# Kernel tuning notes

Hardware: AMD Instinct MI355X
Metric: run time of the kernel (lower is better)

## Reference

```python
import jax, jax.numpy as jnp
import numpy as np

B, S, D, H = 2, 2048, 1024, 16
HD = D // H  # head_size = 64

def setup_inputs() -> dict:
    key = jax.random.key(0)
    ks = jax.random.split(key, 8)
    sc = 0.02
    return {
        "q": jax.random.normal(ks[0], (B, S, D), jnp.float32),
        "k": jax.random.normal(ks[1], (B, S, D), jnp.float32),
        "v": jax.random.normal(ks[2], (B, S, D), jnp.float32),
        "padding_mask": jnp.zeros((B, 1, 1, S), jnp.float32),
        "Wq": jax.random.normal(ks[3], (D, D), jnp.float32) * sc,
        "bq": jnp.zeros((D,), jnp.float32),
        "Wk": jax.random.normal(ks[4], (D, D), jnp.float32) * sc,
        "bk": jnp.zeros((D,), jnp.float32),
        "Wv": jax.random.normal(ks[5], (D, D), jnp.float32) * sc,
        "bv": jnp.zeros((D,), jnp.float32),
        "Wo": jax.random.normal(ks[6], (D, D), jnp.float32) * sc,
        "bo": jnp.zeros((D,), jnp.float32),
    }

def reference(q, k, v, padding_mask, Wq, bq, Wk, bk, Wv, bv, Wo, bo):
    b = q.shape[0]
    qh = (q @ Wq + bq).reshape(b, -1, H, HD)
    kh = (k @ Wk + bk).reshape(b, -1, H, HD)
    vh = (v @ Wv + bv).reshape(b, -1, H, HD)
    # [B, H, Sq, Sk] scores, materialized as in the original
    qk = jnp.einsum('bjhd,bkhd->bhjk', qh, kh) / jnp.sqrt(jnp.float32(HD))
    qk = qk + padding_mask * -1e12
    attn = jax.nn.softmax(qk, axis=-1)
    qkv = jnp.einsum('bhjk,bkhd->bjhd', attn, vh).reshape(b, -1, D)
    return qkv @ Wo + bo
```

## Files before the change

### kernel.cpp

```cpp
#include <hip/hip_runtime.h>
#include <math.h>

typedef __bf16 bf16_t;
typedef __bf16 bf16x8 __attribute__((ext_vector_type(8)));
typedef __bf16 bf16x4v __attribute__((ext_vector_type(4)));
typedef float f32x4 __attribute__((ext_vector_type(4)));
typedef float f32x16 __attribute__((ext_vector_type(16)));

#define LOG2E 1.4426950408889634f
#define MBIAS_C (-1e12f * LOG2E)

#if __has_builtin(__builtin_amdgcn_exp2f)
#define EXP2F(x) __builtin_amdgcn_exp2f(x)
#else
#define EXP2F(x) exp2f(x)
#endif

typedef __attribute__((address_space(1))) const unsigned int g_u32;
typedef __attribute__((address_space(3))) unsigned int l_u32;
__device__ __forceinline__ void load_lds_16B(const void* g, void* l){
  __builtin_amdgcn_global_load_lds((g_u32*)g, (l_u32*)l, 16, 0, 0);
}

__device__ __forceinline__ f32x16 zero16(){
  f32x16 z;
  #pragma unroll
  for (int i = 0; i < 16; i++) z[i] = 0.f;
  return z;
}

__global__ __launch_bounds__(256) void cast3_kernel(const float* __restrict__ q,
                                                    const float* __restrict__ k,
                                                    const float* __restrict__ v,
                                                    bf16_t* __restrict__ out){
  int z = blockIdx.y;
  const float* x = (z == 0) ? q : (z == 1) ? k : v;
  int i = blockIdx.x * 256 + threadIdx.x;
  float4 f = reinterpret_cast<const float4*>(x)[i];
  bf16x4v w;
  w[0] = (bf16_t)f.x; w[1] = (bf16_t)f.y; w[2] = (bf16_t)f.z; w[3] = (bf16_t)f.w;
  reinterpret_cast<bf16x4v*>(out + (size_t)z * 4194304)[i] = w;
}

__global__ __launch_bounds__(256) void wtrans4_kernel(const float* __restrict__ Wq,
                                                      const float* __restrict__ Wk,
                                                      const float* __restrict__ Wv,
                                                      const float* __restrict__ Wo,
                                                      bf16_t* __restrict__ Wcat,
                                                      bf16_t* __restrict__ Wot){
  __shared__ float T[32][33];
  int z = blockIdx.z;
  const float* W = (z == 0) ? Wq : (z == 1) ? Wk : (z == 2) ? Wv : Wo;
  bf16_t* dst = (z < 3) ? (Wcat + (size_t)z * 1024 * 1024) : Wot;
  int x = threadIdx.x, y = threadIdx.y;
  int k0 = blockIdx.y * 32, n0 = blockIdx.x * 32;
  #pragma unroll
  for (int i = 0; i < 4; i++) T[y + 8*i][x] = W[(size_t)(k0 + y + 8*i) * 1024 + n0 + x];
  __syncthreads();
  #pragma unroll
  for (int i = 0; i < 4; i++) dst[(size_t)(n0 + y + 8*i) * 1024 + k0 + x] = (bf16_t)T[x][y + 8*i];
}

__device__ __forceinline__ void qkv_epilogue(f32x4 (&acc)[4][4], int seg, int n0g, int m0,
                                             int wm, int wn, int l16, int lq,
                                             const float* bias, bf16_t* qp, bf16_t* kp,
                                             bf16_t* Vt){
  if (seg < 2){
    bf16_t* Cp = (seg == 0) ? qp : kp;
    float scale = (seg == 0) ? 0.125f * LOG2E : 1.0f;
    #pragma unroll
    for (int ti = 0; ti < 4; ti++){
      #pragma unroll
      for (int tj = 0; tj < 4; tj++){
        int col = (n0g + wn + tj*16 + l16) & 1023;
        float bvv = bias[col];
        #pragma unroll
        for (int r = 0; r < 4; r++){
          int row = m0 + wm + ti*16 + lq*4 + r;
          Cp[(size_t)row * 1024 + col] = (bf16_t)((acc[ti][tj][r] + bvv) * scale);
        }
      }
    }
  } else {
    #pragma unroll
    for (int ti = 0; ti < 4; ti++){
      #pragma unroll
      for (int tj = 0; tj < 4; tj++){
        int dg = (n0g - 2048) + wn + tj*16 + l16;
        int h = dg >> 6, dl = dg & 63;
        float bvv = bias[dg];
        #pragma unroll
        for (int r = 0; r < 4; r++){
          int row = m0 + wm + ti*16 + lq*4 + r;
          int b = row >> 11, s = row & 2047;
          Vt[(size_t)((b*16 + h)*64 + dl) * 2048 + s] = (bf16_t)(acc[ti][tj][r] + bvv);
        }
      }
    }
  }
}

__global__ __launch_bounds__(256) void gemm_qkv_bf(const bf16_t* __restrict__ qkvin,
                                                   const bf16_t* __restrict__ Wcat,
                                                   const float* __restrict__ bq,
                                                   const float* __restrict__ bk,
                                                   const float* __restrict__ bv,
                                                   bf16_t* __restrict__ qp,
                                                   bf16_t* __restrict__ kp,
                                                   bf16_t* __restrict__ Vt){
  const int K = 1024;
  __shared__ __align__(16) bf16_t As[128*32];
  __shared__ __align__(16) bf16_t Bs[128*32];
  int tid = threadIdx.x, wave = tid >> 6, lane = tid & 63;
  int l16 = lane & 15, lq = lane >> 4;
  int n0g = blockIdx.x * 128;
  int seg = n0g >> 10;
  const bf16_t* A   = qkvin + (size_t)seg * 4194304;
  const float* bias = (seg == 0) ? bq : (seg == 1) ? bk : bv;
  int m0 = blockIdx.y * 128;
  int wm = (wave >> 1) * 64, wn = (wave & 1) * 64;
  int cposR = lq ^ ((l16 >> 2) & 3);
  f32x4 acc[4][4] = {};
  for (int kt = 0; kt < K; kt += 32){
    __syncthreads();
    #pragma unroll
    for (int i = 0; i < 2; i++){
      int u = tid + 256*i;
      int r = u >> 2, cpos = u & 3, cg = cpos ^ ((r >> 2) & 3);
      int ldsoff = (wave*64 + 256*i) * 16;
      load_lds_16B(&A[(size_t)(m0 + r) * K + kt + cg*8], (char*)As + ldsoff);
      load_lds_16B(&Wcat[(size_t)(n0g + r) * K + kt + cg*8], (char*)Bs + ldsoff);
    }
    __syncthreads();
    bf16x8 af[4], bfr[4];
    #pragma unroll
    for (int t = 0; t < 4; t++) af[t]  = *reinterpret_cast<bf16x8*>(&As[(wm + t*16 + l16)*32 + cposR*8]);
    #pragma unroll
    for (int t = 0; t < 4; t++) bfr[t] = *reinterpret_cast<bf16x8*>(&Bs[(wn + t*16 + l16)*32 + cposR*8]);
    #pragma unroll
    for (int ti = 0; ti < 4; ti++)
      #pragma unroll
      for (int tj = 0; tj < 4; tj++)
        acc[ti][tj] = __builtin_amdgcn_mfma_f32_16x16x32_bf16(af[ti], bfr[tj], acc[ti][tj], 0, 0, 0);
  }
  qkv_epilogue(acc, seg, n0g, m0, wm, wn, l16, lq, bias, qp, kp, Vt);
}

__global__ __launch_bounds__(256) void gemm_qkv_f32(const float* __restrict__ qi,
                                                    const float* __restrict__ ki,
                                                    const float* __restrict__ vi,
                                                    const bf16_t* __restrict__ Wcat,
                                                    const float* __restrict__ bq,
                                                    const float* __restrict__ bk,
                                                    const float* __restrict__ bv,
                                                    bf16_t* __restrict__ qp,
                                                    bf16_t* __restrict__ kp,
                                                    bf16_t* __restrict__ Vt){
  const int K = 1024;
  __shared__ __align__(16) float  Asf[128*32];
  __shared__ __align__(16) bf16_t Bs[128*32];
  int tid = threadIdx.x, wave = tid >> 6, lane = tid & 63;
  int l16 = lane & 15, lq = lane >> 4;
  int n0g = blockIdx.x * 128;
  int seg = n0g >> 10;
  const float* A    = (seg == 0) ? qi : (seg == 1) ? ki : vi;
  const float* bias = (seg == 0) ? bq : (seg == 1) ? bk : bv;
  int m0 = blockIdx.y * 128;
  int wm = (wave >> 1) * 64, wn = (wave & 1) * 64;
  int cposR = lq ^ ((l16 >> 2) & 3);
  int ca0 = (2*lq)     ^ (l16 & 7);
  int ca1 = (2*lq + 1) ^ (l16 & 7);
  f32x4 acc[4][4] = {};
  for (int kt = 0; kt < K; kt += 32){
    __syncthreads();
    #pragma unroll
    for (int i = 0; i < 4; i++){
      int u = tid + 256*i;
      int r = u >> 3, cpos = u & 7, cg = cpos ^ (r & 7);
      load_lds_16B(&A[(size_t)(m0 + r) * K + kt + cg*4], (char*)Asf + (wave*64 + 256*i)*16);
    }
    #pragma unroll
    for (int i = 0; i < 2; i++){
      int u = tid + 256*i;
      int r = u >> 2, cpos = u & 3, cg = cpos ^ ((r >> 2) & 3);
      load_lds_16B(&Wcat[(size_t)(n0g + r) * K + kt + cg*8], (char*)Bs + (wave*64 + 256*i)*16);
    }
    __syncthreads();
    bf16x8 af[4], bfr[4];
    #pragma unroll
    for (int t = 0; t < 4; t++){
      int row = wm + t*16 + l16;
      f32x4 x0 = *reinterpret_cast<f32x4*>(&Asf[row*32 + ca0*4]);
      f32x4 x1 = *reinterpret_cast<f32x4*>(&Asf[row*32 + ca1*4]);
      bf16x8 a;
      a[0] = (bf16_t)x0[0]; a[1] = (bf16_t)x0[1]; a[2] = (bf16_t)x0[2]; a[3] = (bf16_t)x0[3];
      a[4] = (bf16_t)x1[0]; a[5] = (bf16_t)x1[1]; a[6] = (bf16_t)x1[2]; a[7] = (bf16_t)x1[3];
      af[t] = a;
    }
    #pragma unroll
    for (int t = 0; t < 4; t++) bfr[t] = *reinterpret_cast<bf16x8*>(&Bs[(wn + t*16 + l16)*32 + cposR*8]);
    #pragma unroll
    for (int ti = 0; ti < 4; ti++)
      #pragma unroll
      for (int tj = 0; tj < 4; tj++)
        acc[ti][tj] = __builtin_amdgcn_mfma_f32_16x16x32_bf16(af[ti], bfr[tj], acc[ti][tj], 0, 0, 0);
  }
  qkv_epilogue(acc, seg, n0g, m0, wm, wn, l16, lq, bias, qp, kp, Vt);
}

__global__ __launch_bounds__(256) void gemm_out(const bf16_t* __restrict__ A,
                                                const bf16_t* __restrict__ Bt,
                                                const float* __restrict__ bias,
                                                float* __restrict__ C){
  const int K = 1024, N = 1024;
  __shared__ __align__(16) bf16_t As[128*64];
  __shared__ __align__(16) bf16_t Bs[64*64];
  int tid = threadIdx.x, wave = tid >> 6, lane = tid & 63;
  int l16 = lane & 15, lq = lane >> 4;
  int m0 = blockIdx.y * 128, n0 = blockIdx.x * 64;
  int wm = wave * 32;
  f32x4 acc[2][4] = {};
  for (int kt = 0; kt < K; kt += 64){
    __syncthreads();
    #pragma unroll
    for (int i = 0; i < 4; i++){
      int u = tid + 256*i;
      int r = u >> 3, cpos = u & 7, cg = cpos ^ (r & 7);
      load_lds_16B(&A[(size_t)(m0 + r) * K + kt + cg*8], (char*)As + (wave*64 + 256*i)*16);
    }
    #pragma unroll
    for (int i = 0; i < 2; i++){
      int u = tid + 256*i;
      int r = u >> 3, cpos = u & 7, cg = cpos ^ (r & 7);
      load_lds_16B(&Bt[(size_t)(n0 + r) * K + kt + cg*8], (char*)Bs + (wave*64 + 256*i)*16);
    }
    __syncthreads();
    #pragma unroll
    for (int kk = 0; kk < 2; kk++){
      bf16x8 af[2], bfr[4];
      #pragma unroll
      for (int t = 0; t < 2; t++){
        int row = wm + t*16 + l16, cpos = (kk*4 + lq) ^ (l16 & 7);
        af[t] = *reinterpret_cast<bf16x8*>(&As[row*64 + cpos*8]);
      }
      #pragma unroll
      for (int t = 0; t < 4; t++){
        int row = t*16 + l16, cpos = (kk*4 + lq) ^ (l16 & 7);
        bfr[t] = *reinterpret_cast<bf16x8*>(&Bs[row*64 + cpos*8]);
      }
      #pragma unroll
      for (int ti = 0; ti < 2; ti++)
        #pragma unroll
        for (int tj = 0; tj < 4; tj++)
          acc[ti][tj] = __builtin_amdgcn_mfma_f32_16x16x32_bf16(af[ti], bfr[tj], acc[ti][tj], 0, 0, 0);
    }
  }
  #pragma unroll
  for (int ti = 0; ti < 2; ti++){
    #pragma unroll
    for (int tj = 0; tj < 4; tj++){
      int col = n0 + tj*16 + l16;
      float bvv = bias[col];
      #pragma unroll
      for (int r = 0; r < 4; r++){
        int row = m0 + wm + ti*16 + lq*4 + r;
        C[(size_t)row * N + col] = acc[ti][tj][r] + bvv;
      }
    }
  }
}

__global__ __launch_bounds__(256) void attn_kernel(const bf16_t* __restrict__ qp,
                                                   const bf16_t* __restrict__ kp,
                                                   const bf16_t* __restrict__ vt,
                                                   const float* __restrict__ mask,
                                                   bf16_t* __restrict__ ctx){
  const int S = 2048, D = 1024, HD = 64;
  __shared__ __align__(16) char smem[26624];
  bf16_t* Qs   = (bf16_t*)smem;
  bf16_t* Ps   = (bf16_t*)smem;
  bf16_t* Ks   = (bf16_t*)(smem + 10240);
  bf16_t* Vts  = (bf16_t*)(smem + 18432);
  float* Opart = (float*)smem;
  float* Lsum  = (float*)(smem + 16384);
  float* Lcomb = (float*)(smem + 16640);
  int tid = threadIdx.x, wave = tid >> 6, lane = tid & 63;
  int l32 = lane & 31, H = lane >> 5;
  int qhalf = wave & 1, khalf = wave >> 1;
  int qt = blockIdx.x, h = blockIdx.y, b = blockIdx.z;
  const bf16_t* Qg = qp + (size_t)b*S*D + h*HD;
  const bf16_t* Kg = kp + (size_t)b*S*D + h*HD;
  const bf16_t* Vg = vt + (size_t)(b*16 + h)*HD*S;

  #pragma unroll
  for (int i = 0; i < 2; i++){
    int u = tid + 256*i;
    int r = u >> 3, c = u & 7, cg = c ^ (r & 7);
    load_lds_16B(&Qg[(size_t)(qt*64 + r) * D + cg*8], smem + (wave*64 + 256*i)*16);
  }
  __syncthreads();
  int qrow = qhalf*32 + l32;
  bf16x8 qf[4];
  #pragma unroll
  for (int s = 0; s < 4; s++){
    int c = 2*s + H;
    qf[s] = *reinterpret_cast<bf16x8*>(&Qs[qrow*64 + (c ^ (qrow & 7))*8]);
  }
  f32x16 o0 = zero16(), o1 = zero16();
  float lacc = 0.f;
  int krow = khalf*32 + l32;
  bf16_t* Pw = Ps + wave*32*40;

  for (int kt = 0; kt < S; kt += 64){
    __syncthreads();
    #pragma unroll
    for (int i = 0; i < 2; i++){
      int u = tid + 256*i;
      int r = u >> 3, c = u & 7, cg = c ^ (r & 7);
      load_lds_16B(&Kg[(size_t)(kt + r) * D + cg*8], (char*)Ks + (wave*64 + 256*i)*16);
    }
    #pragma unroll
    for (int i = 0; i < 2; i++){
      int u = tid + 256*i;
      int r = u >> 3, c = u & 7, cg = c ^ (r & 7);
      load_lds_16B(&Vg[(size_t)r * S + kt + cg*8], (char*)Vts + (wave*64 + 256*i)*16);
    }
    __syncthreads();

    f32x16 sc;
    #pragma unroll
    for (int s = 0; s < 4; s++){
      int c = 2*s + H;
      bf16x8 kf = *reinterpret_cast<bf16x8*>(&Ks[krow*64 + (c ^ (krow & 7))*8]);
      if (s == 0) sc = __builtin_amdgcn_mfma_f32_32x32x16_bf16(kf, qf[0], zero16(), 0, 0, 0);
      else        sc = __builtin_amdgcn_mfma_f32_32x32x16_bf16(kf, qf[s], sc, 0, 0, 0);
    }
    float lt = 0.f;
    #pragma unroll
    for (int g = 0; g < 4; g++){
      int kcol = kt + khalf*32 + 8*g + 4*H;
      float4 mv = *reinterpret_cast<const float4*>(&mask[(size_t)b*S + kcol]);
      float p0 = EXP2F(fmaf(mv.x, MBIAS_C, sc[4*g+0]));
      float p1 = EXP2F(fmaf(mv.y, MBIAS_C, sc[4*g+1]));
      float p2 = EXP2F(fmaf(mv.z, MBIAS_C, sc[4*g+2]));
      float p3 = EXP2F(fmaf(mv.w, MBIAS_C, sc[4*g+3]));
      lt += (p0 + p1) + (p2 + p3);
      bf16x4v w;
      w[0] = (bf16_t)p0; w[1] = (bf16_t)p1; w[2] = (bf16_t)p2; w[3] = (bf16_t)p3;
      *reinterpret_cast<bf16x4v*>(&Pw[l32*40 + 8*g + 4*H]) = w;
    }
    lt += __shfl_xor(lt, 32);
    lacc += lt;
    #pragma unroll
    for (int ks = 0; ks < 2; ks++){
      bf16x8 pf = *reinterpret_cast<bf16x8*>(&Pw[l32*40 + ks*16 + 8*H]);
      int c0 = 4*khalf + 2*ks + H;
      bf16x8 vf0 = *reinterpret_cast<bf16x8*>(&Vts[l32*64 + (c0 ^ (l32 & 7))*8]);
      bf16x8 vf1 = *reinterpret_cast<bf16x8*>(&Vts[(32 + l32)*64 + (c0 ^ (l32 & 7))*8]);
      o0 = __builtin_amdgcn_mfma_f32_32x32x16_bf16(pf, vf0, o0, 0, 0, 0);
      o1 = __builtin_amdgcn_mfma_f32_32x32x16_bf16(pf, vf1, o1, 0, 0, 0);
    }
  }
  __syncthreads();
  if (khalf == 1){
    #pragma unroll
    for (int reg = 0; reg < 16; reg++){
      Opart[qhalf*2048 + reg*64 + lane]        = o0[reg];
      Opart[qhalf*2048 + 1024 + reg*64 + lane] = o1[reg];
    }
    Lsum[qhalf*32 + l32] = lacc;
  }
  __syncthreads();
  if (khalf == 0){
    #pragma unroll
    for (int reg = 0; reg < 16; reg++){
      o0[reg] += Opart[qhalf*2048 + reg*64 + lane];
      o1[reg] += Opart[qhalf*2048 + 1024 + reg*64 + lane];
    }
    lacc += Lsum[qhalf*32 + l32];
    Lcomb[qhalf*32 + l32] = lacc;
    #pragma unroll
    for (int g = 0; g < 4; g++){
      f32x4 lv = *reinterpret_cast<f32x4*>(&Lcomb[qhalf*32 + 8*g + 4*H]);
      #pragma unroll
      for (int j = 0; j < 4; j++){
        float inv = 1.f / lv[j];
        int grow = qt*64 + qhalf*32 + 8*g + 4*H + j;
        size_t base = (size_t)(b*S + grow) * D + h*HD;
        ctx[base + l32]      = (bf16_t)(o0[4*g + j] * inv);
        ctx[base + 32 + l32] = (bf16_t)(o1[4*g + j] * inv);
      }
    }
  }
}

extern "C" void kernel_launch(void* const* d_in, const int* in_sizes, int n_in,
                              void* d_out, int out_size, void* d_ws, size_t ws_size,
                              hipStream_t stream){
  const float* q    = (const float*)d_in[0];
  const float* k    = (const float*)d_in[1];
  const float* v    = (const float*)d_in[2];
  const float* mask = (const float*)d_in[3];
  const float* Wq   = (const float*)d_in[4];
  const float* bq   = (const float*)d_in[5];
  const float* Wk   = (const float*)d_in[6];
  const float* bk   = (const float*)d_in[7];
  const float* Wv   = (const float*)d_in[8];
  const float* bv   = (const float*)d_in[9];
  const float* Wo   = (const float*)d_in[10];
  const float* bo   = (const float*)d_in[11];

  char* ws = (char*)d_ws;
  bf16_t* qp    = (bf16_t*)(ws);
  bf16_t* kp    = (bf16_t*)(ws + 8388608);
  bf16_t* Vt    = (bf16_t*)(ws + 16777216);
  bf16_t* Wcat  = (bf16_t*)(ws + 25165824);
  bf16_t* Wot   = (bf16_t*)(ws + 31457280);
  bf16_t* ctx   = (bf16_t*)(ws + 33554432);
  bf16_t* qkvin = (bf16_t*)(ws + 33554432);

  wtrans4_kernel<<<dim3(32,32,4), dim3(32,8), 0, stream>>>(Wq, Wk, Wv, Wo, Wcat, Wot);
  if (ws_size >= 58720256){
    cast3_kernel<<<dim3(4096,3), 256, 0, stream>>>(q, k, v, qkvin);
    gemm_qkv_bf<<<dim3(24,32), 256, 0, stream>>>(qkvin, Wcat, bq, bk, bv, qp, kp, Vt);
  } else {
    gemm_qkv_f32<<<dim3(24,32), 256, 0, stream>>>(q, k, v, Wcat, bq, bk, bv, qp, kp, Vt);
  }
  attn_kernel<<<dim3(32,16,2), 256, 0, stream>>>(qp, kp, Vt, mask, ctx);
  gemm_out<<<dim3(16,32), 256, 0, stream>>>(ctx, Wot, bo, (float*)d_out);
}
```

Baseline: 268.7 us.

## Restructure attention to 128-row Q tiles with register-resident P and separate V transpose

The attention kernel now gives each wave 32 query rows against the full 64-key tile, instead of splitting keys across wave pairs. This removes the cross-wave O reduction through LDS, and P is rebuilt in registers with lane shuffles instead of a round trip through LDS. Q fragments load straight from global memory, and the grid halves to 16 query tiles of 128 rows. The scattered transposed V store in the QKV GEMM epilogue is replaced by a plain row-major store followed by a new LDS-tiled transpose kernel. That adds an extra launch and an extra pass over V in exchange for coalesced writes, and the fewer, larger attention blocks may lower occupancy.

```diff
diff --git a/kernel.cpp b/kernel.cpp
--- a/kernel.cpp
+++ b/kernel.cpp
@@ -28,6 +28,9 @@
   for (int i = 0; i < 16; i++) z[i] = 0.f;
   return z;
 }
+
+typedef union { bf16x4v b4; uint2 u2; } pk8;
+typedef union { uint2 h[2]; bf16x8 b8; } pk16;
 
 __global__ __launch_bounds__(256) void cast3_kernel(const float* __restrict__ q,
                                                     const float* __restrict__ k,
@@ -64,37 +67,19 @@
 __device__ __forceinline__ void qkv_epilogue(f32x4 (&acc)[4][4], int seg, int n0g, int m0,
                                              int wm, int wn, int l16, int lq,
                                              const float* bias, bf16_t* qp, bf16_t* kp,
-                                             bf16_t* Vt){
-  if (seg < 2){
-    bf16_t* Cp = (seg == 0) ? qp : kp;
-    float scale = (seg == 0) ? 0.125f * LOG2E : 1.0f;
-    #pragma unroll
-    for (int ti = 0; ti < 4; ti++){
-      #pragma unroll
-      for (int tj = 0; tj < 4; tj++){
-        int col = (n0g + wn + tj*16 + l16) & 1023;
-        float bvv = bias[col];
-        #pragma unroll
-        for (int r = 0; r < 4; r++){
-          int row = m0 + wm + ti*16 + lq*4 + r;
-          Cp[(size_t)row * 1024 + col] = (bf16_t)((acc[ti][tj][r] + bvv) * scale);
-        }
-      }
-    }
-  } else {
-    #pragma unroll
-    for (int ti = 0; ti < 4; ti++){
-      #pragma unroll
-      for (int tj = 0; tj < 4; tj++){
-        int dg = (n0g - 2048) + wn + tj*16 + l16;
-        int h = dg >> 6, dl = dg & 63;
-        float bvv = bias[dg];
-        #pragma unroll
-        for (int r = 0; r < 4; r++){
-          int row = m0 + wm + ti*16 + lq*4 + r;
-          int b = row >> 11, s = row & 2047;
-          Vt[(size_t)((b*16 + h)*64 + dl) * 2048 + s] = (bf16_t)(acc[ti][tj][r] + bvv);
-        }
+                                             bf16_t* vh){
+  bf16_t* Cp = (seg == 0) ? qp : (seg == 1) ? kp : vh;
+  float scale = (seg == 0) ? 0.125f * LOG2E : 1.0f;
+  #pragma unroll
+  for (int ti = 0; ti < 4; ti++){
+    #pragma unroll
+    for (int tj = 0; tj < 4; tj++){
+      int col = (n0g + wn + tj*16 + l16) & 1023;
+      float bvv = bias[col];
+      #pragma unroll
+      for (int r = 0; r < 4; r++){
+        int row = m0 + wm + ti*16 + lq*4 + r;
+        Cp[(size_t)row * 1024 + col] = (bf16_t)((acc[ti][tj][r] + bvv) * scale);
       }
     }
   }
@@ -107,7 +92,7 @@
                                                    const float* __restrict__ bv,
                                                    bf16_t* __restrict__ qp,
                                                    bf16_t* __restrict__ kp,
-                                                   bf16_t* __restrict__ Vt){
+                                                   bf16_t* __restrict__ vh){
   const int K = 1024;
   __shared__ __align__(16) bf16_t As[128*32];
   __shared__ __align__(16) bf16_t Bs[128*32];
@@ -143,7 +128,7 @@
       for (int tj = 0; tj < 4; tj++)
         acc[ti][tj] = __builtin_amdgcn_mfma_f32_16x16x32_bf16(af[ti], bfr[tj], acc[ti][tj], 0, 0, 0);
   }
-  qkv_epilogue(acc, seg, n0g, m0, wm, wn, l16, lq, bias, qp, kp, Vt);
+  qkv_epilogue(acc, seg, n0g, m0, wm, wn, l16, lq, bias, qp, kp, vh);
 }
 
 __global__ __launch_bounds__(256) void gemm_qkv_f32(const float* __restrict__ qi,
@@ -155,7 +140,7 @@
                                                     const float* __restrict__ bv,
                                                     bf16_t* __restrict__ qp,
                                                     bf16_t* __restrict__ kp,
-                                                    bf16_t* __restrict__ Vt){
+                                                    bf16_t* __restrict__ vh){
   const int K = 1024;
   __shared__ __align__(16) float  Asf[128*32];
   __shared__ __align__(16) bf16_t Bs[128*32];
@@ -205,7 +190,7 @@
       for (int tj = 0; tj < 4; tj++)
         acc[ti][tj] = __builtin_amdgcn_mfma_f32_16x16x32_bf16(af[ti], bfr[tj], acc[ti][tj], 0, 0, 0);
   }
-  qkv_epilogue(acc, seg, n0g, m0, wm, wn, l16, lq, bias, qp, kp, Vt);
+  qkv_epilogue(acc, seg, n0g, m0, wm, wn, l16, lq, bias, qp, kp, vh);
 }
 
 __global__ __launch_bounds__(256) void gemm_out(const bf16_t* __restrict__ A,
@@ -270,46 +255,56 @@
   }
 }
 
+__global__ __launch_bounds__(256) void vtrans_kernel(const bf16_t* __restrict__ vh,
+                                                     bf16_t* __restrict__ Vt){
+  __shared__ bf16_t T[64][72];
+  int tid = threadIdx.x;
+  int s0 = blockIdx.x * 64, h = blockIdx.y, b = blockIdx.z;
+  #pragma unroll
+  for (int i = 0; i < 2; i++){
+    int u = tid + 256*i;
+    int r = u >> 3, c = (u & 7) * 8;
+    *reinterpret_cast<uint4*>(&T[r][c]) =
+      *reinterpret_cast<const uint4*>(&vh[(size_t)(b*2048 + s0 + r) * 1024 + h*64 + c]);
+  }
+  __syncthreads();
+  #pragma unroll
+  for (int i = 0; i < 2; i++){
+    int u = tid + 256*i;
+    int d = u >> 3, cs = (u & 7) * 8;
+    bf16_t t8[8];
+    #pragma unroll
+    for (int j = 0; j < 8; j++) t8[j] = T[cs + j][d];
+    *reinterpret_cast<uint4*>(&Vt[(size_t)((b*16 + h)*64 + d) * 2048 + s0 + cs]) =
+      *reinterpret_cast<uint4*>(t8);
+  }
+}
+
 __global__ __launch_bounds__(256) void attn_kernel(const bf16_t* __restrict__ qp,
                                                    const bf16_t* __restrict__ kp,
                                                    const bf16_t* __restrict__ vt,
                                                    const float* __restrict__ mask,
                                                    bf16_t* __restrict__ ctx){
   const int S = 2048, D = 1024, HD = 64;
-  __shared__ __align__(16) char smem[26624];
-  bf16_t* Qs   = (bf16_t*)smem;
-  bf16_t* Ps   = (bf16_t*)smem;
-  bf16_t* Ks   = (bf16_t*)(smem + 10240);
-  bf16_t* Vts  = (bf16_t*)(smem + 18432);
-  float* Opart = (float*)smem;
-  float* Lsum  = (float*)(smem + 16384);
-  float* Lcomb = (float*)(smem + 16640);
+  __shared__ __align__(16) char smem[16896];
+  bf16_t* Ks  = (bf16_t*)smem;
+  bf16_t* Vts = (bf16_t*)(smem + 8192);
+  float* Lbuf = (float*)(smem + 16384);
   int tid = threadIdx.x, wave = tid >> 6, lane = tid & 63;
   int l32 = lane & 31, H = lane >> 5;
-  int qhalf = wave & 1, khalf = wave >> 1;
   int qt = blockIdx.x, h = blockIdx.y, b = blockIdx.z;
   const bf16_t* Qg = qp + (size_t)b*S*D + h*HD;
   const bf16_t* Kg = kp + (size_t)b*S*D + h*HD;
   const bf16_t* Vg = vt + (size_t)(b*16 + h)*HD*S;
 
-  #pragma unroll
-  for (int i = 0; i < 2; i++){
-    int u = tid + 256*i;
-    int r = u >> 3, c = u & 7, cg = c ^ (r & 7);
-    load_lds_16B(&Qg[(size_t)(qt*64 + r) * D + cg*8], smem + (wave*64 + 256*i)*16);
-  }
-  __syncthreads();
-  int qrow = qhalf*32 + l32;
+  int qrow = qt*128 + wave*32 + l32;
   bf16x8 qf[4];
   #pragma unroll
-  for (int s = 0; s < 4; s++){
-    int c = 2*s + H;
-    qf[s] = *reinterpret_cast<bf16x8*>(&Qs[qrow*64 + (c ^ (qrow & 7))*8]);
-  }
+  for (int s = 0; s < 4; s++)
+    qf[s] = *reinterpret_cast<const bf16x8*>(&Qg[(size_t)qrow * D + s*16 + 8*H]);
+
   f32x16 o0 = zero16(), o1 = zero16();
   float lacc = 0.f;
-  int krow = khalf*32 + l32;
-  bf16_t* Pw = Ps + wave*32*40;
 
   for (int kt = 0; kt < S; kt += 64){
     __syncthreads();
@@ -327,69 +322,69 @@
     }
     __syncthreads();
 
-    f32x16 sc;
+    f32x16 sc0, sc1;
     #pragma unroll
     for (int s = 0; s < 4; s++){
-      int c = 2*s + H;
-      bf16x8 kf = *reinterpret_cast<bf16x8*>(&Ks[krow*64 + (c ^ (krow & 7))*8]);
-      if (s == 0) sc = __builtin_amdgcn_mfma_f32_32x32x16_bf16(kf, qf[0], zero16(), 0, 0, 0);
-      else        sc = __builtin_amdgcn_mfma_f32_32x32x16_bf16(kf, qf[s], sc, 0, 0, 0);
-    }
-    float lt = 0.f;
-    #pragma unroll
-    for (int g = 0; g < 4; g++){
-      int kcol = kt + khalf*32 + 8*g + 4*H;
-      float4 mv = *reinterpret_cast<const float4*>(&mask[(size_t)b*S + kcol]);
-      float p0 = EXP2F(fmaf(mv.x, MBIAS_C, sc[4*g+0]));
-      float p1 = EXP2F(fmaf(mv.y, MBIAS_C, sc[4*g+1]));
-      float p2 = EXP2F(fmaf(mv.z, MBIAS_C, sc[4*g+2]));
-      float p3 = EXP2F(fmaf(mv.w, MBIAS_C, sc[4*g+3]));
-      lt += (p0 + p1) + (p2 + p3);
-      bf16x4v w;
-      w[0] = (bf16_t)p0; w[1] = (bf16_t)p1; w[2] = (bf16_t)p2; w[3] = (bf16_t)p3;
-      *reinterpret_cast<bf16x4v*>(&Pw[l32*40 + 8*g + 4*H]) = w;
-    }
-    lt += __shfl_xor(lt, 32);
-    lacc += lt;
-    #pragma unroll
-    for (int ks = 0; ks < 2; ks++){
-      bf16x8 pf = *reinterpret_cast<bf16x8*>(&Pw[l32*40 + ks*16 + 8*H]);
-      int c0 = 4*khalf + 2*ks + H;
-      bf16x8 vf0 = *reinterpret_cast<bf16x8*>(&Vts[l32*64 + (c0 ^ (l32 & 7))*8]);
-      bf16x8 vf1 = *reinterpret_cast<bf16x8*>(&Vts[(32 + l32)*64 + (c0 ^ (l32 & 7))*8]);
-      o0 = __builtin_amdgcn_mfma_f32_32x32x16_bf16(pf, vf0, o0, 0, 0, 0);
-      o1 = __builtin_amdgcn_mfma_f32_32x32x16_bf16(pf, vf1, o1, 0, 0, 0);
-    }
-  }
-  __syncthreads();
-  if (khalf == 1){
-    #pragma unroll
-    for (int reg = 0; reg < 16; reg++){
-      Opart[qhalf*2048 + reg*64 + lane]        = o0[reg];
-      Opart[qhalf*2048 + 1024 + reg*64 + lane] = o1[reg];
-    }
-    Lsum[qhalf*32 + l32] = lacc;
-  }
-  __syncthreads();
-  if (khalf == 0){
-    #pragma unroll
-    for (int reg = 0; reg < 16; reg++){
-      o0[reg] += Opart[qhalf*2048 + reg*64 + lane];
-      o1[reg] += Opart[qhalf*2048 + 1024 + reg*64 + lane];
-    }
-    lacc += Lsum[qhalf*32 + l32];
-    Lcomb[qhalf*32 + l32] = lacc;
-    #pragma unroll
-    for (int g = 0; g < 4; g++){
-      f32x4 lv = *reinterpret_cast<f32x4*>(&Lcomb[qhalf*32 + 8*g + 4*H]);
-      #pragma unroll
-      for (int j = 0; j < 4; j++){
-        float inv = 1.f / lv[j];
-        int grow = qt*64 + qhalf*32 + 8*g + 4*H + j;
-        size_t base = (size_t)(b*S + grow) * D + h*HD;
-        ctx[base + l32]      = (bf16_t)(o0[4*g + j] * inv);
-        ctx[base + 32 + l32] = (bf16_t)(o1[4*g + j] * inv);
-      }
+      int cp = (2*s + H) ^ (l32 & 7);
+      bf16x8 kf0 = *reinterpret_cast<bf16x8*>(&Ks[l32*64 + cp*8]);
+      bf16x8 kf1 = *reinterpret_cast<bf16x8*>(&Ks[(32 + l32)*64 + cp*8]);
+      if (s == 0){
+        sc0 = __builtin_amdgcn_mfma_f32_32x32x16_bf16(kf0, qf[0], zero16(), 0, 0, 0);
+        sc1 = __builtin_amdgcn_mfma_f32_32x32x16_bf16(kf1, qf[0], zero16(), 0, 0, 0);
+      } else {
+        sc0 = __builtin_amdgcn_mfma_f32_32x32x16_bf16(kf0, qf[s], sc0, 0, 0, 0);
+        sc1 = __builtin_amdgcn_mfma_f32_32x32x16_bf16(kf1, qf[s], sc1, 0, 0, 0);
+      }
+    }
+    pk8 grp[2][4];
+    #pragma unroll
+    for (int t = 0; t < 2; t++){
+      const f32x16& s = t ? sc1 : sc0;
+      #pragma unroll
+      for (int g = 0; g < 4; g++){
+        int kcol = kt + t*32 + 8*g + 4*H;
+        float4 mv = *reinterpret_cast<const float4*>(&mask[(size_t)b*S + kcol]);
+        float p0 = EXP2F(fmaf(mv.x, MBIAS_C, s[4*g+0]));
+        float p1 = EXP2F(fmaf(mv.y, MBIAS_C, s[4*g+1]));
+        float p2 = EXP2F(fmaf(mv.z, MBIAS_C, s[4*g+2]));
+        float p3 = EXP2F(fmaf(mv.w, MBIAS_C, s[4*g+3]));
+        lacc += (p0 + p1) + (p2 + p3);
+        pk8 w;
+        w.b4[0] = (bf16_t)p0; w.b4[1] = (bf16_t)p1; w.b4[2] = (bf16_t)p2; w.b4[3] = (bf16_t)p3;
+        grp[t][g] = w;
+      }
+    }
+    #pragma unroll
+    for (int kk = 0; kk < 4; kk++){
+      int t = kk >> 1, w = kk & 1;
+      uint2 ga = grp[t][2*w].u2;
+      uint2 gb = grp[t][2*w+1].u2;
+      uint2 send = H ? ga : gb;
+      uint2 recv;
+      recv.x = (unsigned)__shfl_xor((int)send.x, 32);
+      recv.y = (unsigned)__shfl_xor((int)send.y, 32);
+      pk16 fr;
+      fr.h[0] = H ? recv : ga;
+      fr.h[1] = H ? gb : recv;
+      int cp = (2*kk + H) ^ (l32 & 7);
+      bf16x8 vf0 = *reinterpret_cast<bf16x8*>(&Vts[l32*64 + cp*8]);
+      bf16x8 vf1 = *reinterpret_cast<bf16x8*>(&Vts[(32 + l32)*64 + cp*8]);
+      o0 = __builtin_amdgcn_mfma_f32_32x32x16_bf16(fr.b8, vf0, o0, 0, 0, 0);
+      o1 = __builtin_amdgcn_mfma_f32_32x32x16_bf16(fr.b8, vf1, o1, 0, 0, 0);
+    }
+  }
+  float lfull = lacc + __shfl_xor(lacc, 32);
+  Lbuf[wave*32 + l32] = lfull;
+  #pragma unroll
+  for (int g = 0; g < 4; g++){
+    f32x4 lv = *reinterpret_cast<f32x4*>(&Lbuf[wave*32 + 8*g + 4*H]);
+    #pragma unroll
+    for (int r = 0; r < 4; r++){
+      float inv = 1.f / lv[r];
+      int grow = qt*128 + wave*32 + 8*g + 4*H + r;
+      size_t base = (size_t)(b*S + grow) * D + h*HD;
+      ctx[base + l32]      = (bf16_t)(o0[4*g + r] * inv);
+      ctx[base + 32 + l32] = (bf16_t)(o1[4*g + r] * inv);
     }
   }
 }
@@ -413,19 +408,21 @@
   char* ws = (char*)d_ws;
   bf16_t* qp    = (bf16_t*)(ws);
   bf16_t* kp    = (bf16_t*)(ws + 8388608);
-  bf16_t* Vt    = (bf16_t*)(ws + 16777216);
+  bf16_t* vh    = (bf16_t*)(ws + 16777216);
   bf16_t* Wcat  = (bf16_t*)(ws + 25165824);
   bf16_t* Wot   = (bf16_t*)(ws + 31457280);
-  bf16_t* ctx   = (bf16_t*)(ws + 33554432);
+  bf16_t* Vt    = (bf16_t*)(ws + 33554432);
+  bf16_t* ctx   = (bf16_t*)(ws + 41943040);
   bf16_t* qkvin = (bf16_t*)(ws + 33554432);
 
   wtrans4_kernel<<<dim3(32,32,4), dim3(32,8), 0, stream>>>(Wq, Wk, Wv, Wo, Wcat, Wot);
   if (ws_size >= 58720256){
     cast3_kernel<<<dim3(4096,3), 256, 0, stream>>>(q, k, v, qkvin);
-    gemm_qkv_bf<<<dim3(24,32), 256, 0, stream>>>(qkvin, Wcat, bq, bk, bv, qp, kp, Vt);
+    gemm_qkv_bf<<<dim3(24,32), 256, 0, stream>>>(qkvin, Wcat, bq, bk, bv, qp, kp, vh);
   } else {
-    gemm_qkv_f32<<<dim3(24,32), 256, 0, stream>>>(q, k, v, Wcat, bq, bk, bv, qp, kp, Vt);
-  }
-  attn_kernel<<<dim3(32,16,2), 256, 0, stream>>>(qp, kp, Vt, mask, ctx);
+    gemm_qkv_f32<<<dim3(24,32), 256, 0, stream>>>(q, k, v, Wcat, bq, bk, bv, qp, kp, vh);
+  }
+  vtrans_kernel<<<dim3(32,16,2), 256, 0, stream>>>(vh, Vt);
+  attn_kernel<<<dim3(16,16,2), 256, 0, stream>>>(qp, kp, Vt, mask, ctx);
   gemm_out<<<dim3(16,32), 256, 0, stream>>>(ctx, Wot, bo, (float*)d_out);
 }
```

Result: no change. 263.8 us (-1.8%).
